# Kernel tuning notes

Measured on AMD Instinct MI355X. Metric: run time of the kernel, lower is better.

Reference implementation:

```python
import jax, jax.numpy as jnp
import numpy as np

# AlphaFold2-scale config
C_S, C_Z, H, D = 256, 128, 8, 32
T = H * D  # total_dim = 256
B, S, N = 1, 128, 256  # batch, MSA rows, residues
EPS = 1e-5
SCALE = 1.0 / np.sqrt(D).astype(np.float32)


def _layer_norm(x, w, b):
    m = jnp.mean(x, axis=-1, keepdims=True)
    v = jnp.var(x, axis=-1, keepdims=True)
    return (x - m) * jax.lax.rsqrt(v + EPS) * w + b


def setup_inputs() -> dict:
    key = jax.random.key(0)
    ks = jax.random.split(key, 8)
    w = lambda k, shape: jax.random.normal(k, shape, dtype=jnp.float32) * 0.02
    return {
        "msa_representation": jax.random.normal(ks[0], (B, S, N, C_S), dtype=jnp.float32),
        "pair_representation": jax.random.normal(ks[1], (B, N, N, C_Z), dtype=jnp.float32),
        "ln_msa_w": jnp.ones((C_S,), jnp.float32),
        "ln_msa_b": jnp.zeros((C_S,), jnp.float32),
        "ln_pair_w": jnp.ones((C_Z,), jnp.float32),
        "ln_pair_b": jnp.zeros((C_Z,), jnp.float32),
        "Wq": w(ks[2], (C_S, T)),
        "Wk": w(ks[3], (C_S, T)),
        "Wv": w(ks[4], (C_S, T)),
        "Wpair": w(ks[5], (C_Z, H)),
        "Wg": w(ks[6], (C_S, T)),
        "bg": jnp.zeros((T,), jnp.float32),
        "Wo": w(ks[7], (T, C_S)),
        "bo": jnp.zeros((C_S,), jnp.float32),
    }


def reference(msa_representation, pair_representation, ln_msa_w, ln_msa_b,
              ln_pair_w, ln_pair_b, Wq, Wk, Wv, Wpair, Wg, bg, Wo, bo):
    msa = _layer_norm(msa_representation, ln_msa_w, ln_msa_b)  # [B,S,N,C_S]
    q = (msa @ Wq).reshape(B, S, N, H, D)
    k = (msa @ Wk).reshape(B, S, N, H, D)
    v = (msa @ Wv).reshape(B, S, N, H, D)
    g = jax.nn.sigmoid(msa @ Wg + bg).reshape(B, S, N, H, D)

    pair = _layer_norm(pair_representation, ln_pair_w, ln_pair_b)  # [B,N,N,C_Z]
    bias = jnp.transpose(pair @ Wpair, (0, 3, 1, 2))[:, None]  # [B,1,H,N,N]

    scores = jnp.einsum('bsihd,bsjhd->bshij', q, k) * SCALE + bias  # [B,S,H,N,N]
    attn = jax.nn.softmax(scores, axis=-1)
    vals = jnp.einsum('bshij,bsjhd->bsihd', attn, v)  # [B,S,N,H,D]
    vals = (g * vals).reshape(B, S, N, T)
    return vals @ Wo + bo  # [B,S,N,C_S]
```

## Files before the change

### kernel.cpp

```cpp
#include <hip/hip_runtime.h>

typedef unsigned short u16;
typedef unsigned int u32;
typedef __bf16 bf16x8 __attribute__((ext_vector_type(8)));
typedef float f32x4 __attribute__((ext_vector_type(4)));

#define EPS 1e-5f
#define SCALE 0.17677669529663687f

__device__ __forceinline__ u16 f2bf(float f) {
  u32 u = __builtin_bit_cast(u32, f);
  u32 r = (u + 0x7fffu + ((u >> 16) & 1u)) >> 16;
  return (u16)r;
}
__device__ __forceinline__ float bf2f(u16 v) {
  return __builtin_bit_cast(float, (u32)v << 16);
}
__device__ __forceinline__ u32 pack2(float a, float b) {
  return (u32)f2bf(a) | ((u32)f2bf(b) << 16);
}

__global__ __launch_bounds__(256) void k_ln_msa(const float* __restrict__ x,
                                                const float* __restrict__ w,
                                                const float* __restrict__ b,
                                                u16* __restrict__ y) {
  int wid = threadIdx.x >> 6, lane = threadIdx.x & 63;
  long row = (long)blockIdx.x * 4 + wid;
  const float4 v = *reinterpret_cast<const float4*>(x + row * 256 + lane * 4);
  float s = v.x + v.y + v.z + v.w;
  float ss = v.x * v.x + v.y * v.y + v.z * v.z + v.w * v.w;
#pragma unroll
  for (int off = 1; off < 64; off <<= 1) {
    s += __shfl_xor(s, off);
    ss += __shfl_xor(ss, off);
  }
  float m = s * (1.0f / 256.0f);
  float var = ss * (1.0f / 256.0f) - m * m;
  float rs = rsqrtf(var + EPS);
  int c = lane * 4;
  u16 o0 = f2bf((v.x - m) * rs * w[c + 0] + b[c + 0]);
  u16 o1 = f2bf((v.y - m) * rs * w[c + 1] + b[c + 1]);
  u16 o2 = f2bf((v.z - m) * rs * w[c + 2] + b[c + 2]);
  u16 o3 = f2bf((v.w - m) * rs * w[c + 3] + b[c + 3]);
  uint2 pk;
  pk.x = (u32)o0 | ((u32)o1 << 16);
  pk.y = (u32)o2 | ((u32)o3 << 16);
  *reinterpret_cast<uint2*>(y + row * 256 + c) = pk;
}

__global__ __launch_bounds__(256) void k_pair_bias(const float* __restrict__ x,
                                                   const float* __restrict__ w,
                                                   const float* __restrict__ b,
                                                   const float* __restrict__ Wp,
                                                   float* __restrict__ bias) {
  int wid = threadIdx.x >> 6, lane = threadIdx.x & 63;
  long row = (long)blockIdx.x * 4 + wid;
  const float2 v = *reinterpret_cast<const float2*>(x + row * 128 + lane * 2);
  float s = v.x + v.y, ss = v.x * v.x + v.y * v.y;
#pragma unroll
  for (int off = 1; off < 64; off <<= 1) {
    s += __shfl_xor(s, off);
    ss += __shfl_xor(ss, off);
  }
  float m = s * (1.0f / 128.0f);
  float var = ss * (1.0f / 128.0f) - m * m;
  float rs = rsqrtf(var + EPS);
  int c = lane * 2;
  float x0 = (v.x - m) * rs * w[c] + b[c];
  float x1 = (v.y - m) * rs * w[c + 1] + b[c + 1];
  const float4* wp = reinterpret_cast<const float4*>(Wp + (long)c * 8);
  float4 a0 = wp[0], a1 = wp[1], a2 = wp[2], a3 = wp[3];
  float p[8];
  p[0] = x0 * a0.x + x1 * a2.x; p[1] = x0 * a0.y + x1 * a2.y;
  p[2] = x0 * a0.z + x1 * a2.z; p[3] = x0 * a0.w + x1 * a2.w;
  p[4] = x0 * a1.x + x1 * a3.x; p[5] = x0 * a1.y + x1 * a3.y;
  p[6] = x0 * a1.z + x1 * a3.z; p[7] = x0 * a1.w + x1 * a3.w;
#pragma unroll
  for (int off = 1; off < 64; off <<= 1) {
#pragma unroll
    for (int h = 0; h < 8; h++) p[h] += __shfl_xor(p[h], off);
  }
  if (lane == 0) {
#pragma unroll
    for (int h = 0; h < 8; h++) bias[(long)h * 65536 + row] = p[h];
  }
}

__global__ __launch_bounds__(256) void k_prep_w(const float* __restrict__ Wq,
                                                const float* __restrict__ Wk,
                                                const float* __restrict__ Wv,
                                                const float* __restrict__ Wg,
                                                const float* __restrict__ Wo,
                                                u16* __restrict__ Wt,
                                                u16* __restrict__ WoT) {
  int tid = blockIdx.x * 256 + threadIdx.x;
  if (tid < 262144) {
    int n = tid >> 8, kk = tid & 255;
    int sel = n >> 8, c = n & 255;
    const float* W = (sel == 0) ? Wq : (sel == 1) ? Wk : (sel == 2) ? Wv : Wg;
    float v = W[kk * 256 + c];
    if (sel == 0) v *= SCALE;
    Wt[tid] = f2bf(v);
  } else {
    int t = tid - 262144;
    int n = t >> 8, kk = t & 255;
    WoT[t] = f2bf(Wo[kk * 256 + n]);
  }
}

__global__ __launch_bounds__(256) void k_proj(const u16* __restrict__ X,
                                              const u16* __restrict__ Wt,
                                              const float* __restrict__ bg,
                                              u16* __restrict__ qkg,
                                              u16* __restrict__ vt) {
  __shared__ u16 Bs[128 * 256];
  int tid = threadIdx.x;
  int wid = tid >> 6, lane = tid & 63;
  int lr = lane & 15, lg = lane >> 4;
  int m0 = blockIdx.x * 128;
  int n0 = blockIdx.y * 128;
  int sel = n0 >> 8;

#pragma unroll
  for (int i = 0; i < 16; i++) {
    int u = i * 256 + tid;
    int n = u >> 5, cu = u & 31;
    uint4 xw = *reinterpret_cast<const uint4*>(Wt + (long)(n0 + n) * 256 + cu * 8);
    *reinterpret_cast<uint4*>(&Bs[n * 256 + ((cu ^ (n & 7)) * 8)]) = xw;
  }
  __syncthreads();

  int mw = m0 + wid * 32;
  bf16x8 a[2][8];
#pragma unroll
  for (int mi = 0; mi < 2; mi++)
#pragma unroll
    for (int kk = 0; kk < 8; kk++)
      a[mi][kk] = *reinterpret_cast<const bf16x8*>(
          X + (long)(mw + mi * 16 + lr) * 256 + kk * 32 + lg * 8);

  f32x4 acc[2][8];
#pragma unroll
  for (int mi = 0; mi < 2; mi++)
#pragma unroll
    for (int ni = 0; ni < 8; ni++) acc[mi][ni] = (f32x4){0.f, 0.f, 0.f, 0.f};

#pragma unroll
  for (int ni = 0; ni < 8; ni++) {
    bf16x8 bfr[8];
#pragma unroll
    for (int kk = 0; kk < 8; kk++)
      bfr[kk] = *reinterpret_cast<const bf16x8*>(
          &Bs[(ni * 16 + lr) * 256 + (((kk * 4 + lg) ^ (lr & 7)) * 8)]);
#pragma unroll
    for (int kk = 0; kk < 8; kk++) {
      acc[0][ni] = __builtin_amdgcn_mfma_f32_16x16x32_bf16(a[0][kk], bfr[kk], acc[0][ni], 0, 0, 0);
      acc[1][ni] = __builtin_amdgcn_mfma_f32_16x16x32_bf16(a[1][kk], bfr[kk], acc[1][ni], 0, 0, 0);
    }
  }

  int s = m0 >> 8;
  if (sel == 2) {
#pragma unroll
    for (int ni = 0; ni < 8; ni++) {
      int cq = (n0 & 255) + ni * 16 + lr;
      int hh = cq >> 5, dd = cq & 31;
      u16* vbase = vt + (((long)s * 8 + hh) * 32 + dd) * 256;
#pragma unroll
      for (int mi = 0; mi < 2; mi++) {
        int i = (m0 & 255) + wid * 32 + mi * 16 + lg * 4;
        uint2 pk;
        pk.x = pack2(acc[mi][ni][0], acc[mi][ni][1]);
        pk.y = pack2(acc[mi][ni][2], acc[mi][ni][3]);
        *reinterpret_cast<uint2*>(vbase + i) = pk;
      }
    }
  } else {
    int t = (sel == 3) ? 2 : sel;
#pragma unroll
    for (int ni = 0; ni < 8; ni++) {
      int cq = (n0 & 255) + ni * 16 + lr;
      int hh = cq >> 5, dd = cq & 31;
      float bgv = (sel == 3) ? bg[cq] : 0.f;
      u16* qbase = qkg + (long)(t * 8 + hh) * 32768 * 32;
#pragma unroll
      for (int mi = 0; mi < 2; mi++) {
#pragma unroll
        for (int r = 0; r < 4; r++) {
          int row = m0 + wid * 32 + mi * 16 + lg * 4 + r;
          float val = acc[mi][ni][r];
          if (sel == 3) val = 1.0f / (1.0f + __expf(-(val + bgv)));
          qbase[(long)row * 32 + dd] = f2bf(val);
        }
      }
    }
  }
}

__global__ __launch_bounds__(256) void k_attn(const u16* __restrict__ qkg,
                                              const u16* __restrict__ vt,
                                              const float* __restrict__ bias,
                                              u16* __restrict__ vals) {
  __shared__ alignas(16) u16 VTs[32 * 256];
  __shared__ alignas(16) u16 Plds[4][16 * 128];
  int tid = threadIdx.x;
  int wid = tid >> 6, lane = tid & 63;
  int lr = lane & 15, lg = lane >> 4;
  int h = blockIdx.x, s = blockIdx.y;

  const u16* qb = qkg + ((long)(0 + h) * 32768 + s * 256) * 32;
  const u16* kb = qkg + ((long)(8 + h) * 32768 + s * 256) * 32;
  const u16* gb = qkg + ((long)(16 + h) * 32768 + s * 256) * 32;
  const u16* vb = vt + ((long)s * 8 + h) * 32 * 256;

#pragma unroll
  for (int k = 0; k < 4; k++) {
    int c = tid + k * 256;
    uint4 vu = *reinterpret_cast<const uint4*>(vb + c * 8);
    int d = c >> 5, pp = c & 31;
    *reinterpret_cast<uint4*>(&VTs[d * 256 + ((pp ^ (d & 7)) * 8)]) = vu;
  }
  __syncthreads();

  for (int ig = 0; ig < 4; ig++) {
    int iw0 = wid * 64 + ig * 16;
    bf16x8 qf = *reinterpret_cast<const bf16x8*>(qb + (long)(iw0 + lr) * 32 + lg * 8);

    f32x4 p[16];
#pragma unroll
    for (int jt = 0; jt < 16; jt++) {
      bf16x8 kf = *reinterpret_cast<const bf16x8*>(kb + (long)(jt * 16 + lr) * 32 + lg * 8);
      f32x4 z = (f32x4){0.f, 0.f, 0.f, 0.f};
      p[jt] = __builtin_amdgcn_mfma_f32_16x16x32_bf16(kf, qf, z, 0, 0, 0);
    }

    const float4* bp4 =
        reinterpret_cast<const float4*>(bias + (long)h * 65536 + (long)(iw0 + lr) * 256);
    float sum = 0.f;
    f32x4 o[2];
    o[0] = (f32x4){0.f, 0.f, 0.f, 0.f};
    o[1] = (f32x4){0.f, 0.f, 0.f, 0.f};

#pragma unroll
    for (int half = 0; half < 2; half++) {
#pragma unroll
      for (int jt8 = 0; jt8 < 8; jt8++) {
        int jt = half * 8 + jt8;
        float4 bv = bp4[jt * 4 + lg];
        float e0 = __expf(p[jt][0] + bv.x);
        float e1 = __expf(p[jt][1] + bv.y);
        float e2 = __expf(p[jt][2] + bv.z);
        float e3 = __expf(p[jt][3] + bv.w);
        sum += (e0 + e1) + (e2 + e3);
        int u = (jt8 * 2 + (lg >> 1)) ^ (lr & 7);
        uint2 pk;
        pk.x = pack2(e0, e1);
        pk.y = pack2(e2, e3);
        *reinterpret_cast<uint2*>(&Plds[wid][lr * 128 + u * 8 + (lg & 1) * 4]) = pk;
      }
#pragma unroll
      for (int ks4 = 0; ks4 < 4; ks4++) {
        int ks = half * 4 + ks4;
        int pu = (ks4 * 4 + lg) ^ (lr & 7);
        bf16x8 pa = *reinterpret_cast<const bf16x8*>(&Plds[wid][lr * 128 + pu * 8]);
#pragma unroll
        for (int nt = 0; nt < 2; nt++) {
          int vu = (ks * 4 + lg) ^ (lr & 7);
          bf16x8 vf = *reinterpret_cast<const bf16x8*>(&VTs[(nt * 16 + lr) * 256 + vu * 8]);
          o[nt] = __builtin_amdgcn_mfma_f32_16x16x32_bf16(vf, pa, o[nt], 0, 0, 0);
        }
      }
    }

    sum += __shfl_xor(sum, 16);
    sum += __shfl_xor(sum, 32);

    float inv = 1.0f / sum;
    int row = iw0 + lr;
#pragma unroll
    for (int nt = 0; nt < 2; nt++) {
      int d0 = nt * 16 + lg * 4;
      uint2 gv = *reinterpret_cast<const uint2*>(gb + (long)row * 32 + d0);
      float g0 = bf2f((u16)(gv.x & 0xffff)), g1 = bf2f((u16)(gv.x >> 16));
      float g2 = bf2f((u16)(gv.y & 0xffff)), g3 = bf2f((u16)(gv.y >> 16));
      uint2 st;
      st.x = pack2(o[nt][0] * inv * g0, o[nt][1] * inv * g1);
      st.y = pack2(o[nt][2] * inv * g2, o[nt][3] * inv * g3);
      *reinterpret_cast<uint2*>(&vals[((long)s * 256 + row) * 256 + h * 32 + d0]) = st;
    }
  }
}

__global__ __launch_bounds__(256) void k_out(const u16* __restrict__ X,
                                             const u16* __restrict__ WoT,
                                             const float* __restrict__ bo,
                                             float* __restrict__ out) {
  __shared__ u16 Bs[128 * 256];
  int tid = threadIdx.x;
  int wid = tid >> 6, lane = tid & 63;
  int lr = lane & 15, lg = lane >> 4;
  int m0 = blockIdx.x * 128;
  int n0 = blockIdx.y * 128;

#pragma unroll
  for (int i = 0; i < 16; i++) {
    int u = i * 256 + tid;
    int n = u >> 5, cu = u & 31;
    uint4 xw = *reinterpret_cast<const uint4*>(WoT + (long)(n0 + n) * 256 + cu * 8);
    *reinterpret_cast<uint4*>(&Bs[n * 256 + ((cu ^ (n & 7)) * 8)]) = xw;
  }
  __syncthreads();

  int mw = m0 + wid * 32;
  bf16x8 a[2][8];
#pragma unroll
  for (int mi = 0; mi < 2; mi++)
#pragma unroll
    for (int kk = 0; kk < 8; kk++)
      a[mi][kk] = *reinterpret_cast<const bf16x8*>(
          X + (long)(mw + mi * 16 + lr) * 256 + kk * 32 + lg * 8);

  f32x4 acc[2][8];
#pragma unroll
  for (int mi = 0; mi < 2; mi++)
#pragma unroll
    for (int ni = 0; ni < 8; ni++) acc[mi][ni] = (f32x4){0.f, 0.f, 0.f, 0.f};

#pragma unroll
  for (int ni = 0; ni < 8; ni++) {
    bf16x8 bfr[8];
#pragma unroll
    for (int kk = 0; kk < 8; kk++)
      bfr[kk] = *reinterpret_cast<const bf16x8*>(
          &Bs[(ni * 16 + lr) * 256 + (((kk * 4 + lg) ^ (lr & 7)) * 8)]);
#pragma unroll
    for (int kk = 0; kk < 8; kk++) {
      acc[0][ni] = __builtin_amdgcn_mfma_f32_16x16x32_bf16(a[0][kk], bfr[kk], acc[0][ni], 0, 0, 0);
      acc[1][ni] = __builtin_amdgcn_mfma_f32_16x16x32_bf16(a[1][kk], bfr[kk], acc[1][ni], 0, 0, 0);
    }
  }

#pragma unroll
  for (int ni = 0; ni < 8; ni++) {
    int col = n0 + ni * 16 + lr;
    float bias_c = bo[col];
#pragma unroll
    for (int mi = 0; mi < 2; mi++) {
#pragma unroll
      for (int r = 0; r < 4; r++) {
        int row = m0 + wid * 32 + mi * 16 + lg * 4 + r;
        out[(long)row * 256 + col] = acc[mi][ni][r] + bias_c;
      }
    }
  }
}

extern "C" void kernel_launch(void* const* d_in, const int* in_sizes, int n_in,
                              void* d_out, int out_size, void* d_ws, size_t ws_size,
                              hipStream_t stream) {
  (void)in_sizes; (void)n_in; (void)out_size; (void)ws_size;
  const float* msa = (const float*)d_in[0];
  const float* pair = (const float*)d_in[1];
  const float* ln_msa_w = (const float*)d_in[2];
  const float* ln_msa_b = (const float*)d_in[3];
  const float* ln_pair_w = (const float*)d_in[4];
  const float* ln_pair_b = (const float*)d_in[5];
  const float* Wq = (const float*)d_in[6];
  const float* Wk = (const float*)d_in[7];
  const float* Wv = (const float*)d_in[8];
  const float* Wpair = (const float*)d_in[9];
  const float* Wg = (const float*)d_in[10];
  const float* bg = (const float*)d_in[11];
  const float* Wo = (const float*)d_in[12];
  const float* bo = (const float*)d_in[13];
  float* out = (float*)d_out;

  char* ws = (char*)d_ws;
  u16* msa_ln = (u16*)(ws + 0);
  u16* qkg    = (u16*)(ws + 16777216);
  u16* vt     = (u16*)(ws + 67108864);
  float* bias = (float*)(ws + 83886080);
  u16* vals   = (u16*)(ws + 85983232);
  u16* Wt     = (u16*)(ws + 102760448);
  u16* WoT    = (u16*)(ws + 103284736);

  k_prep_w<<<dim3(1280), dim3(256), 0, stream>>>(Wq, Wk, Wv, Wg, Wo, Wt, WoT);
  k_ln_msa<<<dim3(8192), dim3(256), 0, stream>>>(msa, ln_msa_w, ln_msa_b, msa_ln);
  k_pair_bias<<<dim3(16384), dim3(256), 0, stream>>>(pair, ln_pair_w, ln_pair_b, Wpair, bias);
  k_proj<<<dim3(256, 8), dim3(256), 0, stream>>>(msa_ln, Wt, bg, qkg, vt);
  k_attn<<<dim3(8, 128), dim3(256), 0, stream>>>(qkg, vt, bias, vals);
  k_out<<<dim3(256, 2), dim3(256), 0, stream>>>(vals, WoT, bo, out);
}
```

Baseline: 174.5 us.

## Split attention query rows across two blocks and stream QK scores in chunks

The attention kernel grid gains a dimension that splits each (s,h) pair's 256 query rows into two blocks of 128, doubling block count from 1024 to 2048. The QK^T MFMAs are now computed in chunks of four key tiles interleaved with exp and PV accumulation, rather than holding all 16 score tiles in registers. The per-wave P staging buffer in LDS shrinks by half. This targets lower register pressure and higher occupancy and parallelism, at the cost of loading the V tile into LDS twice per (s,h).

```diff
diff --git a/kernel.cpp b/kernel.cpp
--- a/kernel.cpp
+++ b/kernel.cpp
@@ -202,11 +202,11 @@
                                               const float* __restrict__ bias,
                                               u16* __restrict__ vals) {
   __shared__ alignas(16) u16 VTs[32 * 256];
-  __shared__ alignas(16) u16 Plds[4][16 * 128];
+  __shared__ alignas(16) u16 Plds[4][16 * 64];
   int tid = threadIdx.x;
   int wid = tid >> 6, lane = tid & 63;
   int lr = lane & 15, lg = lane >> 4;
-  int h = blockIdx.x, s = blockIdx.y;
+  int ihalf = blockIdx.x, h = blockIdx.y, s = blockIdx.z;
 
   const u16* qb = qkg + ((long)(0 + h) * 32768 + s * 256) * 32;
   const u16* kb = qkg + ((long)(8 + h) * 32768 + s * 256) * 32;
@@ -216,53 +216,52 @@
 #pragma unroll
   for (int k = 0; k < 4; k++) {
     int c = tid + k * 256;
-    uint4 vu = *reinterpret_cast<const uint4*>(vb + c * 8);
+    uint4 vu4 = *reinterpret_cast<const uint4*>(vb + c * 8);
     int d = c >> 5, pp = c & 31;
-    *reinterpret_cast<uint4*>(&VTs[d * 256 + ((pp ^ (d & 7)) * 8)]) = vu;
+    *reinterpret_cast<uint4*>(&VTs[d * 256 + ((pp ^ (d & 7)) * 8)]) = vu4;
   }
   __syncthreads();
 
-  for (int ig = 0; ig < 4; ig++) {
-    int iw0 = wid * 64 + ig * 16;
+  for (int ig2 = 0; ig2 < 2; ig2++) {
+    int iw0 = ihalf * 128 + wid * 32 + ig2 * 16;
     bf16x8 qf = *reinterpret_cast<const bf16x8*>(qb + (long)(iw0 + lr) * 32 + lg * 8);
-
-    f32x4 p[16];
-#pragma unroll
-    for (int jt = 0; jt < 16; jt++) {
-      bf16x8 kf = *reinterpret_cast<const bf16x8*>(kb + (long)(jt * 16 + lr) * 32 + lg * 8);
-      f32x4 z = (f32x4){0.f, 0.f, 0.f, 0.f};
-      p[jt] = __builtin_amdgcn_mfma_f32_16x16x32_bf16(kf, qf, z, 0, 0, 0);
-    }
-
     const float4* bp4 =
         reinterpret_cast<const float4*>(bias + (long)h * 65536 + (long)(iw0 + lr) * 256);
+
     float sum = 0.f;
     f32x4 o[2];
     o[0] = (f32x4){0.f, 0.f, 0.f, 0.f};
     o[1] = (f32x4){0.f, 0.f, 0.f, 0.f};
 
 #pragma unroll
-    for (int half = 0; half < 2; half++) {
-#pragma unroll
-      for (int jt8 = 0; jt8 < 8; jt8++) {
-        int jt = half * 8 + jt8;
-        float4 bv = bp4[jt * 4 + lg];
-        float e0 = __expf(p[jt][0] + bv.x);
-        float e1 = __expf(p[jt][1] + bv.y);
-        float e2 = __expf(p[jt][2] + bv.z);
-        float e3 = __expf(p[jt][3] + bv.w);
+    for (int jt4 = 0; jt4 < 4; jt4++) {
+      f32x4 p[4];
+#pragma unroll
+      for (int jj = 0; jj < 4; jj++) {
+        bf16x8 kf = *reinterpret_cast<const bf16x8*>(
+            kb + (long)((jt4 * 4 + jj) * 16 + lr) * 32 + lg * 8);
+        f32x4 z = (f32x4){0.f, 0.f, 0.f, 0.f};
+        p[jj] = __builtin_amdgcn_mfma_f32_16x16x32_bf16(kf, qf, z, 0, 0, 0);
+      }
+#pragma unroll
+      for (int jj = 0; jj < 4; jj++) {
+        float4 bv = bp4[(jt4 * 4 + jj) * 4 + lg];
+        float e0 = __expf(p[jj][0] + bv.x);
+        float e1 = __expf(p[jj][1] + bv.y);
+        float e2 = __expf(p[jj][2] + bv.z);
+        float e3 = __expf(p[jj][3] + bv.w);
         sum += (e0 + e1) + (e2 + e3);
-        int u = (jt8 * 2 + (lg >> 1)) ^ (lr & 7);
+        int u = (jj * 2 + (lg >> 1)) ^ (lr & 7);
         uint2 pk;
         pk.x = pack2(e0, e1);
         pk.y = pack2(e2, e3);
-        *reinterpret_cast<uint2*>(&Plds[wid][lr * 128 + u * 8 + (lg & 1) * 4]) = pk;
-      }
-#pragma unroll
-      for (int ks4 = 0; ks4 < 4; ks4++) {
-        int ks = half * 4 + ks4;
-        int pu = (ks4 * 4 + lg) ^ (lr & 7);
-        bf16x8 pa = *reinterpret_cast<const bf16x8*>(&Plds[wid][lr * 128 + pu * 8]);
+        *reinterpret_cast<uint2*>(&Plds[wid][lr * 64 + u * 8 + (lg & 1) * 4]) = pk;
+      }
+#pragma unroll
+      for (int ksq = 0; ksq < 2; ksq++) {
+        int pu = (ksq * 4 + lg) ^ (lr & 7);
+        bf16x8 pa = *reinterpret_cast<const bf16x8*>(&Plds[wid][lr * 64 + pu * 8]);
+        int ks = jt4 * 2 + ksq;
 #pragma unroll
         for (int nt = 0; nt < 2; nt++) {
           int vu = (ks * 4 + lg) ^ (lr & 7);
@@ -388,6 +387,6 @@
   k_ln_msa<<<dim3(8192), dim3(256), 0, stream>>>(msa, ln_msa_w, ln_msa_b, msa_ln);
   k_pair_bias<<<dim3(16384), dim3(256), 0, stream>>>(pair, ln_pair_w, ln_pair_b, Wpair, bias);
   k_proj<<<dim3(256, 8), dim3(256), 0, stream>>>(msa_ln, Wt, bg, qkg, vt);
-  k_attn<<<dim3(8, 128), dim3(256), 0, stream>>>(qkg, vt, bias, vals);
+  k_attn<<<dim3(2, 8, 128), dim3(256), 0, stream>>>(qkg, vt, bias, vals);
   k_out<<<dim3(256, 2), dim3(256), 0, stream>>>(vals, WoT, bo, out);
 }
```

New measurement: 178.6 us. 1.02x slower.
